# Optimization experiments

Measured on AMD Instinct MI355X. Metric: run time of the kernel, lower is better.

Reference implementation:

```python
import jax, jax.numpy as jnp
import numpy as np


def _conv2d(x, w, b):
    # standard 3x3 conv, stride 1, padding 1, NCHW / OIHW
    y = jax.lax.conv_general_dilated(
        x, w, window_strides=(1, 1), padding=((1, 1), (1, 1)),
        dimension_numbers=('NCHW', 'OIHW', 'NCHW'))
    return y + b[None, :, None, None]


def _deform_conv2d(x, offset, w, b):
    # torchvision deform_conv2d v1 (no modulation mask), 3x3 kernel,
    # stride 1, padding 1, dilation 1.
    N, C, H, W = x.shape
    K = 9  # 3x3 kernel taps
    O = w.shape[0]
    # offset channels: [2k] = dy, [2k+1] = dx for tap k = kh*3 + kw
    off = offset.reshape(N, K, 2, H, W)
    ky = jnp.arange(K) // 3 - 1  # base y displacement per tap (pad=1)
    kx = jnp.arange(K) % 3 - 1   # base x displacement per tap
    # sampling coords [N, K, H, W]
    py = jnp.arange(H)[None, None, :, None] + ky[None, :, None, None] + off[:, :, 0]
    px = jnp.arange(W)[None, None, None, :] + kx[None, :, None, None] + off[:, :, 1]
    y0 = jnp.floor(py)
    x0 = jnp.floor(px)
    dy = py - y0
    dx = px - x0
    y0i = y0.astype(jnp.int32)
    x0i = x0.astype(jnp.int32)
    xf = x.reshape(N, C, H * W)

    def gather(yi, xi):
        # zero-padding outside the image: mask invalid corners
        mask = ((yi >= 0) & (yi < H) & (xi >= 0) & (xi < W)).astype(x.dtype)
        idx = (jnp.clip(yi, 0, H - 1) * W + jnp.clip(xi, 0, W - 1)).reshape(N, -1)
        v = jax.vmap(lambda xn, ix: xn[:, ix])(xf, idx)  # [N, C, K*H*W]
        return v.reshape(N, C, K, H, W) * mask[:, None]

    # bilinear interpolation over 4 corners -> [N, C, K, H, W]
    v = (gather(y0i, x0i) * ((1 - dy) * (1 - dx))[:, None]
         + gather(y0i, x0i + 1) * ((1 - dy) * dx)[:, None]
         + gather(y0i + 1, x0i) * (dy * (1 - dx))[:, None]
         + gather(y0i + 1, x0i + 1) * (dy * dx)[:, None])
    # apply conv weights: implicit GEMM over (c, k)
    out = jnp.einsum('nckhw,ock->nohw', v, w.reshape(O, C, K))
    return out + b[None, :, None, None]


def setup_inputs() -> dict:
    key = jax.random.key(0)
    ks = jax.random.split(key, 4)
    N, C, O, H, W = 8, 128, 128, 80, 80
    fan_in = C * 9
    x = jax.random.normal(ks[0], (N, C, H, W), jnp.float32)
    w_off = jax.random.normal(ks[1], (18, C, 3, 3), jnp.float32) / np.sqrt(fan_in).astype(np.float32)
    b_off = jnp.zeros((18,), jnp.float32)
    w = jax.random.normal(ks[2], (O, C, 3, 3), jnp.float32) / np.sqrt(fan_in).astype(np.float32)
    b = jax.random.normal(ks[3], (O,), jnp.float32) * 0.01
    return {"x": x, "w_off": w_off, "b_off": b_off, "w": w, "b": b}


def reference(x, w_off, b_off, w, b):
    offset = _conv2d(x, w_off, b_off)
    return _deform_conv2d(x, offset, w, b)
```

## Files before the change

### kernel.cpp

```cpp
#include <hip/hip_runtime.h>

#define HWSZ 6400
#define PP   96
#define PLANE (PP*PP*128)
#define VSTR 392

typedef short bf16x8 __attribute__((ext_vector_type(8)));
typedef float f32x4  __attribute__((ext_vector_type(4)));
typedef uint  u32x4  __attribute__((ext_vector_type(4)));

__device__ inline ushort f2bf(float f) {
    uint u = __float_as_uint(f);
    u += 0x7fffu + ((u >> 16) & 1u);
    return (ushort)(u >> 16);
}
__device__ inline float bf2f(ushort u) {
    return __uint_as_float((uint)u << 16);
}
__device__ inline uint pk2(float a, float b) {
    return (uint)f2bf(a) | ((uint)f2bf(b) << 16);
}

__global__ __launch_bounds__(256) void prep_weights(const float* __restrict__ w,
                                                    const float* __restrict__ w_off,
                                                    ushort* __restrict__ wA,
                                                    ushort* __restrict__ wAoff) {
    int idx = blockIdx.x * 256 + threadIdx.x;
    if (idx < 147456) {
        int ot = idx / 18432, rem = idx - ot * 18432;
        int s = rem >> 9, lane = (rem >> 3) & 63, j = rem & 7;
        int o = ot * 16 + (lane & 15);
        int K = s * 32 + 8 * (lane >> 4) + j;
        int k = K >> 7, c = K & 127;
        wA[idx] = f2bf(w[(o * 128 + c) * 9 + k]);
    } else if (idx < 147456 + 36864) {
        int i = idx - 147456;
        int ot = i / 18432, rem = i - ot * 18432;
        int s = rem >> 9, lane = (rem >> 3) & 63, j = rem & 7;
        int o = ot * 16 + (lane & 15);
        int K = s * 32 + 8 * (lane >> 4) + j;
        int k = K >> 7, c = K & 127;
        wAoff[i] = (o < 18) ? f2bf(w_off[(o * 128 + c) * 9 + k]) : (ushort)0;
    }
}

__global__ __launch_bounds__(256) void transpose_x(const float* __restrict__ x,
                                                   ushort* __restrict__ xTp,
                                                   int n_base) {
    __shared__ ushort st[80 * 136];
    int h = blockIdx.x, g = blockIdx.y;
    int t = threadIdx.x;
    const float* xn = x + ((size_t)(n_base + g) * 128) * HWSZ + h * 80;
    for (int i = 0; i < 40; ++i) {
        int e = t + i * 256;
        int c = e / 80;
        int wcol = e - c * 80;
        st[wcol * 136 + c] = f2bf(xn[(size_t)c * HWSZ + wcol]);
    }
    __syncthreads();
    ushort* dst = xTp + (size_t)g * PLANE + ((size_t)(h + 8) * PP + 8) * 128;
    for (int i = 0; i < 5; ++i) {
        int e = t + i * 256;
        int wcol = e >> 4, cq = e & 15;
        u32x4 v = *(const u32x4*)(st + wcol * 136 + cq * 8);
        *(u32x4*)(dst + (size_t)wcol * 128 + cq * 8) = v;
    }
}

__global__ __launch_bounds__(256) void offset_mfma(const ushort* __restrict__ xTp,
                                                   const ushort* __restrict__ wAoff,
                                                   const float* __restrict__ b_off,
                                                   float* __restrict__ offs) {
    __shared__ ushort xs[6 * 18 * 136];
    int t = threadIdx.x;
    int w0 = blockIdx.x * 16, h0 = blockIdx.y * 4, g = blockIdx.z;
    const ushort* xb = xTp + (size_t)g * PLANE + ((size_t)(h0 + 7) * PP + (w0 + 7)) * 128;
    for (int i = 0; i < 7; ++i) {
        int e = t + i * 256;
        if (e < 1728) {
            int r = e / 288, rem = e - r * 288;
            int col = rem >> 4, cq = rem & 15;
            u32x4 v = *(const u32x4*)(xb + ((size_t)r * PP + col) * 128 + cq * 8);
            *(u32x4*)(xs + (r * 18 + col) * 136 + cq * 8) = v;
        }
    }
    __syncthreads();
    int lane = t & 63, wv = t >> 6;
    f32x4 acc0 = {0.f, 0.f, 0.f, 0.f};
    f32x4 acc1 = {0.f, 0.f, 0.f, 0.f};
    #pragma unroll
    for (int k = 0; k < 9; ++k) {
        int ky = k / 3, kx = k - ky * 3;
        #pragma unroll
        for (int q = 0; q < 4; ++q) {
            int s = k * 4 + q;
            bf16x8 a0 = *(const bf16x8*)(wAoff + ((size_t)(0 * 36 + s) * 64 + lane) * 8);
            bf16x8 a1 = *(const bf16x8*)(wAoff + ((size_t)(1 * 36 + s) * 64 + lane) * 8);
            bf16x8 bb = *(const bf16x8*)(xs + ((wv + ky) * 18 + (lane & 15) + kx) * 136
                                          + q * 32 + 8 * (lane >> 4));
            acc0 = __builtin_amdgcn_mfma_f32_16x16x32_bf16(a0, bb, acc0, 0, 0, 0);
            acc1 = __builtin_amdgcn_mfma_f32_16x16x32_bf16(a1, bb, acc1, 0, 0, 0);
        }
    }
    int col = lane & 15, rg = lane >> 4;
    int prow = h0 + wv, pcol = w0 + col;
    #pragma unroll
    for (int r = 0; r < 4; ++r) {
        int oc = rg * 4 + r;
        offs[((size_t)(g * 18 + oc)) * HWSZ + prow * 80 + pcol] = acc0[r] + b_off[oc];
    }
    if (rg == 0) {
        #pragma unroll
        for (int r = 0; r < 2; ++r) {
            int oc = 16 + r;
            offs[((size_t)(g * 18 + oc)) * HWSZ + prow * 80 + pcol] = acc1[r] + b_off[oc];
        }
    }
}

__global__ __launch_bounds__(256) void deform_gemm(const ushort* __restrict__ xTp,
                                                   const float* __restrict__ offs,
                                                   const ushort* __restrict__ wA,
                                                   const float* __restrict__ b,
                                                   float* __restrict__ out,
                                                   int n_base) {
    __shared__ ushort v_lds[32 * VSTR];
    __shared__ int setup[288 * 8];

    int t = threadIdx.x;
    int w0 = blockIdx.x * 16, h0 = blockIdx.y * 2, g = blockIdx.z;
    const ushort* xn = xTp + (size_t)g * PLANE;

    #pragma unroll
    for (int s = 0; s < 2; ++s) {
        int pair = t + s * 256;
        if (pair < 288) {
            int k = pair >> 5, p = pair & 31;
            int hh = h0 + (p >> 4), ww = w0 + (p & 15);
            size_t ob = ((size_t)(g * 18 + 2 * k)) * HWSZ + hh * 80 + ww;
            float dy = offs[ob], dx = offs[ob + HWSZ];
            int ky = k / 3, kx = k - ky * 3;
            float py = fminf(fmaxf((float)(hh + ky - 1) + dy, -7.5f), 86.5f);
            float px = fminf(fmaxf((float)(ww + kx - 1) + dx, -7.5f), 86.5f);
            float y0f = floorf(py), x0f = floorf(px);
            float fy = py - y0f, fx = px - x0f;
            int y0 = (int)y0f + 8, x0 = (int)x0f + 8;
            int rb0 = (y0 * PP + x0) * 128;
            setup[pair * 8 + 0] = rb0;
            setup[pair * 8 + 1] = rb0 + PP * 128;
            ((float*)setup)[pair * 8 + 2] = (1.f - fy) * (1.f - fx);
            ((float*)setup)[pair * 8 + 3] = (1.f - fy) * fx;
            ((float*)setup)[pair * 8 + 4] = fy * (1.f - fx);
            ((float*)setup)[pair * 8 + 5] = fy * fx;
        }
    }
    __syncthreads();

    int lane = t & 63;
    int o_t = (t >> 6) * 2;
    f32x4 acc[2][2];
    #pragma unroll
    for (int oi = 0; oi < 2; ++oi)
        #pragma unroll
        for (int pj = 0; pj < 2; ++pj) {
            f32x4 z = {0.f, 0.f, 0.f, 0.f};
            acc[oi][pj] = z;
        }

    for (int cc = 0; cc < 3; ++cc) {
        if (cc) __syncthreads();
        #pragma unroll
        for (int j = 0; j < 6; ++j) {
            int u = t + j * 256;
            int cg = u & 15;
            int pr = u >> 4;
            int tr = pr >> 5;
            int p  = pr & 31;
            int pair = (cc * 3 + tr) * 32 + p;
            const int* su = &setup[pair * 8];
            int rb0 = su[0], rb1 = su[1];
            float w00 = ((const float*)su)[2], w01 = ((const float*)su)[3];
            float w10 = ((const float*)su)[4], w11 = ((const float*)su)[5];
            const ushort* p0 = xn + rb0 + cg * 8;
            const ushort* p1 = xn + rb1 + cg * 8;
            bf16x8 g00 = *(const bf16x8*)p0;
            bf16x8 g01 = *(const bf16x8*)(p0 + 128);
            bf16x8 g10 = *(const bf16x8*)p1;
            bf16x8 g11 = *(const bf16x8*)(p1 + 128);
            uint r[4];
            #pragma unroll
            for (int c2 = 0; c2 < 4; ++c2) {
                float v0 = w00 * bf2f((ushort)g00[2 * c2])     + w01 * bf2f((ushort)g01[2 * c2])
                         + w10 * bf2f((ushort)g10[2 * c2])     + w11 * bf2f((ushort)g11[2 * c2]);
                float v1 = w00 * bf2f((ushort)g00[2 * c2 + 1]) + w01 * bf2f((ushort)g01[2 * c2 + 1])
                         + w10 * bf2f((ushort)g10[2 * c2 + 1]) + w11 * bf2f((ushort)g11[2 * c2 + 1]);
                r[c2] = pk2(v0, v1);
            }
            u32x4 rv = {r[0], r[1], r[2], r[3]};
            *(u32x4*)(v_lds + p * VSTR + tr * 128 + cg * 8) = rv;
        }
        __syncthreads();
        #pragma unroll
        for (int s = 0; s < 12; ++s) {
            int S = cc * 12 + s;
            bf16x8 a0 = *(const bf16x8*)(wA + ((size_t)(o_t * 36 + S) * 64 + lane) * 8);
            bf16x8 a1 = *(const bf16x8*)(wA + ((size_t)((o_t + 1) * 36 + S) * 64 + lane) * 8);
            const ushort* vb = v_lds + (lane & 15) * VSTR + s * 32 + 8 * (lane >> 4);
            bf16x8 b0 = *(const bf16x8*)vb;
            bf16x8 b1 = *(const bf16x8*)(vb + 16 * VSTR);
            acc[0][0] = __builtin_amdgcn_mfma_f32_16x16x32_bf16(a0, b0, acc[0][0], 0, 0, 0);
            acc[0][1] = __builtin_amdgcn_mfma_f32_16x16x32_bf16(a0, b1, acc[0][1], 0, 0, 0);
            acc[1][0] = __builtin_amdgcn_mfma_f32_16x16x32_bf16(a1, b0, acc[1][0], 0, 0, 0);
            acc[1][1] = __builtin_amdgcn_mfma_f32_16x16x32_bf16(a1, b1, acc[1][1], 0, 0, 0);
        }
    }

    int o_w = (t >> 6) * 32;
    int n = n_base + g;
    #pragma unroll
    for (int oi = 0; oi < 2; ++oi)
        #pragma unroll
        for (int pj = 0; pj < 2; ++pj)
            #pragma unroll
            for (int r = 0; r < 4; ++r) {
                int o = o_w + oi * 16 + (lane >> 4) * 4 + r;
                int col = lane & 15;
                out[((size_t)(n * 128 + o)) * HWSZ + (h0 + pj) * 80 + w0 + col]
                    = acc[oi][pj][r] + b[o];
            }
}

extern "C" void kernel_launch(void* const* d_in, const int* in_sizes, int n_in,
                              void* d_out, int out_size, void* d_ws, size_t ws_size,
                              hipStream_t stream) {
    const float* x     = (const float*)d_in[0];
    const float* w_off = (const float*)d_in[1];
    const float* b_off = (const float*)d_in[2];
    const float* wmain = (const float*)d_in[3];
    const float* bias  = (const float*)d_in[4];
    float* out = (float*)d_out;

    const size_t offsB_full = 8u * 18u * HWSZ * 4u;
    const size_t planeB     = (size_t)PLANE * 2u;
    const bool big = ws_size >= (offsB_full + 8 * planeB + 294912 + 73728);

    if (big) {
        float*  offs  = (float*)d_ws;
        ushort* xTp   = (ushort*)((char*)d_ws + offsB_full);
        ushort* wA    = (ushort*)((char*)xTp + 8 * planeB);
        ushort* wAoff = (ushort*)((char*)wA + 294912);

        hipMemsetAsync(xTp, 0, 8 * planeB, stream);
        prep_weights<<<720, 256, 0, stream>>>(wmain, w_off, wA, wAoff);
        transpose_x<<<dim3(80, 8), 256, 0, stream>>>(x, xTp, 0);
        offset_mfma<<<dim3(5, 20, 8), 256, 0, stream>>>(xTp, wAoff, b_off, offs);
        deform_gemm<<<dim3(5, 40, 8), 256, 0, stream>>>(xTp, offs, wA, bias, out, 0);
    } else {
        ushort* xTp   = (ushort*)d_ws;
        float*  offs  = (float*)((char*)d_ws + planeB);
        ushort* wA    = (ushort*)((char*)offs + 18u * HWSZ * 4u);
        ushort* wAoff = (ushort*)((char*)wA + 294912);

        hipMemsetAsync(xTp, 0, planeB, stream);
        prep_weights<<<720, 256, 0, stream>>>(wmain, w_off, wA, wAoff);
        for (int n = 0; n < 8; ++n) {
            transpose_x<<<dim3(80, 1), 256, 0, stream>>>(x, xTp, n);
            offset_mfma<<<dim3(5, 20, 1), 256, 0, stream>>>(xTp, wAoff, b_off, offs);
            deform_gemm<<<dim3(5, 40, 1), 256, 0, stream>>>(xTp, offs, wA, bias, out, n);
        }
    }
}
```

Baseline: 84.79 us.

## Fuse halo zeroing into transpose, swizzle deform LDS tile, pack bilinear math

The transpose kernel now covers the whole padded 96x96 plane and writes zeros for the halo rows and columns itself, so the separate memset of the padded buffer goes away. In the deform GEMM, the sampled-value LDS tile switches from a padded stride to an unpadded 768-byte row with an XOR swizzle, meant to avoid bank conflicts on the MFMA B-operand reads. The bilinear interpolation now unpacks bf16 pairs with shifts and masks, uses packed two-wide FMAs, and converts with v_cvt_pk_bf16_f32. The trade-offs are extra grid rows of pure zero writes in the transpose and an inline asm dependency.

```diff
diff --git a/kernel.cpp b/kernel.cpp
--- a/kernel.cpp
+++ b/kernel.cpp
@@ -3,22 +3,16 @@
 #define HWSZ 6400
 #define PP   96
 #define PLANE (PP*PP*128)
-#define VSTR 392
 
 typedef short bf16x8 __attribute__((ext_vector_type(8)));
 typedef float f32x4  __attribute__((ext_vector_type(4)));
+typedef float f32x2  __attribute__((ext_vector_type(2)));
 typedef uint  u32x4  __attribute__((ext_vector_type(4)));
 
 __device__ inline ushort f2bf(float f) {
     uint u = __float_as_uint(f);
     u += 0x7fffu + ((u >> 16) & 1u);
     return (ushort)(u >> 16);
-}
-__device__ inline float bf2f(ushort u) {
-    return __uint_as_float((uint)u << 16);
-}
-__device__ inline uint pk2(float a, float b) {
-    return (uint)f2bf(a) | ((uint)f2bf(b) << 16);
 }
 
 __global__ __launch_bounds__(256) void prep_weights(const float* __restrict__ w,
@@ -48,22 +42,28 @@
                                                    ushort* __restrict__ xTp,
                                                    int n_base) {
     __shared__ ushort st[80 * 136];
-    int h = blockIdx.x, g = blockIdx.y;
+    int hp = blockIdx.x, g = blockIdx.y;
     int t = threadIdx.x;
-    const float* xn = x + ((size_t)(n_base + g) * 128) * HWSZ + h * 80;
-    for (int i = 0; i < 40; ++i) {
+    const bool interior = (hp >= 8) && (hp < 88);
+    if (interior) {
+        int h = hp - 8;
+        const float* xn = x + ((size_t)(n_base + g) * 128) * HWSZ + h * 80;
+        for (int i = 0; i < 40; ++i) {
+            int e = t + i * 256;
+            int c = e / 80;
+            int wcol = e - c * 80;
+            st[wcol * 136 + c] = f2bf(xn[(size_t)c * HWSZ + wcol]);
+        }
+        __syncthreads();
+    }
+    ushort* dst = xTp + (size_t)g * PLANE + (size_t)hp * PP * 128;
+    for (int i = 0; i < 6; ++i) {
         int e = t + i * 256;
-        int c = e / 80;
-        int wcol = e - c * 80;
-        st[wcol * 136 + c] = f2bf(xn[(size_t)c * HWSZ + wcol]);
-    }
-    __syncthreads();
-    ushort* dst = xTp + (size_t)g * PLANE + ((size_t)(h + 8) * PP + 8) * 128;
-    for (int i = 0; i < 5; ++i) {
-        int e = t + i * 256;
-        int wcol = e >> 4, cq = e & 15;
-        u32x4 v = *(const u32x4*)(st + wcol * 136 + cq * 8);
-        *(u32x4*)(dst + (size_t)wcol * 128 + cq * 8) = v;
+        int col = e >> 4, cq = e & 15;
+        u32x4 v = {0u, 0u, 0u, 0u};
+        if (interior && col >= 8 && col < 88)
+            v = *(const u32x4*)(st + (col - 8) * 136 + cq * 8);
+        *(u32x4*)(dst + (size_t)col * 128 + cq * 8) = v;
     }
 }
 
@@ -124,7 +124,7 @@
                                                    const float* __restrict__ b,
                                                    float* __restrict__ out,
                                                    int n_base) {
-    __shared__ ushort v_lds[32 * VSTR];
+    __shared__ ushort v_lds[32 * 384];
     __shared__ int setup[288 * 8];
 
     int t = threadIdx.x;
@@ -167,6 +167,10 @@
             acc[oi][pj] = z;
         }
 
+    const int m  = lane & 15;
+    const int q16 = (lane >> 4) * 16;
+    const int xorc = (m & 7) << 4;
+
     for (int cc = 0; cc < 3; ++cc) {
         if (cc) __syncthreads();
         #pragma unroll
@@ -181,23 +185,36 @@
             int rb0 = su[0], rb1 = su[1];
             float w00 = ((const float*)su)[2], w01 = ((const float*)su)[3];
             float w10 = ((const float*)su)[4], w11 = ((const float*)su)[5];
+            f32x2 W00 = {w00, w00}, W01 = {w01, w01};
+            f32x2 W10 = {w10, w10}, W11 = {w11, w11};
             const ushort* p0 = xn + rb0 + cg * 8;
             const ushort* p1 = xn + rb1 + cg * 8;
-            bf16x8 g00 = *(const bf16x8*)p0;
-            bf16x8 g01 = *(const bf16x8*)(p0 + 128);
-            bf16x8 g10 = *(const bf16x8*)p1;
-            bf16x8 g11 = *(const bf16x8*)(p1 + 128);
-            uint r[4];
+            u32x4 g00 = *(const u32x4*)p0;
+            u32x4 g01 = *(const u32x4*)(p0 + 128);
+            u32x4 g10 = *(const u32x4*)p1;
+            u32x4 g11 = *(const u32x4*)(p1 + 128);
+            uint rr[4];
             #pragma unroll
             for (int c2 = 0; c2 < 4; ++c2) {
-                float v0 = w00 * bf2f((ushort)g00[2 * c2])     + w01 * bf2f((ushort)g01[2 * c2])
-                         + w10 * bf2f((ushort)g10[2 * c2])     + w11 * bf2f((ushort)g11[2 * c2]);
-                float v1 = w00 * bf2f((ushort)g00[2 * c2 + 1]) + w01 * bf2f((ushort)g01[2 * c2 + 1])
-                         + w10 * bf2f((ushort)g10[2 * c2 + 1]) + w11 * bf2f((ushort)g11[2 * c2 + 1]);
-                r[c2] = pk2(v0, v1);
+                f32x2 a00 = {__uint_as_float(g00[c2] << 16),
+                             __uint_as_float(g00[c2] & 0xffff0000u)};
+                f32x2 a01 = {__uint_as_float(g01[c2] << 16),
+                             __uint_as_float(g01[c2] & 0xffff0000u)};
+                f32x2 a10 = {__uint_as_float(g10[c2] << 16),
+                             __uint_as_float(g10[c2] & 0xffff0000u)};
+                f32x2 a11 = {__uint_as_float(g11[c2] << 16),
+                             __uint_as_float(g11[c2] & 0xffff0000u)};
+                f32x2 av = a00 * W00;
+                av = __builtin_elementwise_fma(a01, W01, av);
+                av = __builtin_elementwise_fma(a10, W10, av);
+                av = __builtin_elementwise_fma(a11, W11, av);
+                uint pk;
+                asm("v_cvt_pk_bf16_f32 %0, %1, %2" : "=v"(pk) : "v"(av[0]), "v"(av[1]));
+                rr[c2] = pk;
             }
-            u32x4 rv = {r[0], r[1], r[2], r[3]};
-            *(u32x4*)(v_lds + p * VSTR + tr * 128 + cg * 8) = rv;
+            u32x4 rv = {rr[0], rr[1], rr[2], rr[3]};
+            int wb = p * 768 + ((tr * 256 + cg * 16) ^ ((p & 7) << 4));
+            *(u32x4*)((char*)v_lds + wb) = rv;
         }
         __syncthreads();
         #pragma unroll
@@ -205,9 +222,9 @@
             int S = cc * 12 + s;
             bf16x8 a0 = *(const bf16x8*)(wA + ((size_t)(o_t * 36 + S) * 64 + lane) * 8);
             bf16x8 a1 = *(const bf16x8*)(wA + ((size_t)((o_t + 1) * 36 + S) * 64 + lane) * 8);
-            const ushort* vb = v_lds + (lane & 15) * VSTR + s * 32 + 8 * (lane >> 4);
-            bf16x8 b0 = *(const bf16x8*)vb;
-            bf16x8 b1 = *(const bf16x8*)(vb + 16 * VSTR);
+            int rb = m * 768 + ((s * 64 + q16) ^ xorc);
+            bf16x8 b0 = *(const bf16x8*)((const char*)v_lds + rb);
+            bf16x8 b1 = *(const bf16x8*)((const char*)v_lds + rb + 16 * 768);
             acc[0][0] = __builtin_amdgcn_mfma_f32_16x16x32_bf16(a0, b0, acc[0][0], 0, 0, 0);
             acc[0][1] = __builtin_amdgcn_mfma_f32_16x16x32_bf16(a0, b1, acc[0][1], 0, 0, 0);
             acc[1][0] = __builtin_amdgcn_mfma_f32_16x16x32_bf16(a1, b0, acc[1][0], 0, 0, 0);
@@ -250,9 +267,8 @@
         ushort* wA    = (ushort*)((char*)xTp + 8 * planeB);
         ushort* wAoff = (ushort*)((char*)wA + 294912);
 
-        hipMemsetAsync(xTp, 0, 8 * planeB, stream);
         prep_weights<<<720, 256, 0, stream>>>(wmain, w_off, wA, wAoff);
-        transpose_x<<<dim3(80, 8), 256, 0, stream>>>(x, xTp, 0);
+        transpose_x<<<dim3(96, 8), 256, 0, stream>>>(x, xTp, 0);
         offset_mfma<<<dim3(5, 20, 8), 256, 0, stream>>>(xTp, wAoff, b_off, offs);
         deform_gemm<<<dim3(5, 40, 8), 256, 0, stream>>>(xTp, offs, wA, bias, out, 0);
     } else {
@@ -261,10 +277,9 @@
         ushort* wA    = (ushort*)((char*)offs + 18u * HWSZ * 4u);
         ushort* wAoff = (ushort*)((char*)wA + 294912);
 
-        hipMemsetAsync(xTp, 0, planeB, stream);
         prep_weights<<<720, 256, 0, stream>>>(wmain, w_off, wA, wAoff);
         for (int n = 0; n < 8; ++n) {
-            transpose_x<<<dim3(80, 1), 256, 0, stream>>>(x, xTp, n);
+            transpose_x<<<dim3(96, 1), 256, 0, stream>>>(x, xTp, n);
             offset_mfma<<<dim3(5, 20, 1), 256, 0, stream>>>(xTp, wAoff, b_off, offs);
             deform_gemm<<<dim3(5, 40, 1), 256, 0, stream>>>(xTp, offs, wA, bias, out, n);
         }
```

Result: faster. 80.86 us (median of 4 runs) (-4.6%).
